# Optimization experiments

Measured on AMD Instinct MI355X. Metric: run time of the kernel, lower is better.

Reference implementation:

```python
import jax, jax.numpy as jnp
import numpy as np

N_NODES = 10000
N_EDGES = 320000
D = 128
H = 4
C = 128
L = 2
NEG_SLOPE = 0.2
LN_EPS = 1e-5


def setup_inputs() -> dict:
    key = jax.random.key(0)
    ks = jax.random.split(key, 8)
    x = jax.random.normal(ks[0], (N_NODES, D), dtype=jnp.float32)
    edge_index = jax.random.randint(ks[1], (2, N_EDGES), 0, N_NODES, dtype=jnp.int64)
    # weights scaled ~Glorot to keep attention logits in a sane range
    Wl = jax.random.normal(ks[2], (L, D, H * C), dtype=jnp.float32) * 0.1
    Wr = jax.random.normal(ks[3], (L, D, H * C), dtype=jnp.float32) * 0.1
    att = jax.random.normal(ks[4], (L, H, C), dtype=jnp.float32) * 0.1
    return {
        "x": x,
        "edge_index": edge_index,
        "Wl": Wl,
        "bl": jnp.zeros((L, H * C), jnp.float32),
        "Wr": Wr,
        "br": jnp.zeros((L, H * C), jnp.float32),
        "att": att,
        "bias": jnp.zeros((L, D), jnp.float32),
        "ln_g": jnp.ones((L, D), jnp.float32),
        "ln_b": jnp.zeros((L, D), jnp.float32),
    }


def _gatv2_layer(x, src, dst, Wl, bl, Wr, br, att, b):
    """GATv2Conv (concat=False -> head mean), messages src->dst, softmax over dst."""
    n = x.shape[0]
    xl = (x @ Wl + bl).reshape(n, H, C)  # source transform
    xr = (x @ Wr + br).reshape(n, H, C)  # target transform
    s = jax.nn.leaky_relu(xl[src] + xr[dst], NEG_SLOPE)  # [E, H, C]
    e = jnp.einsum("ehc,hc->eh", s, att)  # attention logits [E, H]
    m = jax.ops.segment_max(e, dst, num_segments=n)  # stable softmax per dst segment
    ex = jnp.exp(e - m[dst])
    denom = jax.ops.segment_sum(ex, dst, num_segments=n)
    alpha = ex / denom[dst]  # [E, H]
    out = jax.ops.segment_sum(alpha[:, :, None] * xl[src], dst, num_segments=n)  # [N, H, C]
    return out.mean(axis=1) + b  # concat=False -> mean over heads, then bias


def _layer_norm(h, g, b):
    mu = h.mean(-1, keepdims=True)
    var = ((h - mu) ** 2).mean(-1, keepdims=True)
    return (h - mu) * jax.lax.rsqrt(var + LN_EPS) * g + b


def reference(x, edge_index, Wl, bl, Wr, br, att, bias, ln_g, ln_b):
    n = x.shape[0]
    loop = jnp.arange(n, dtype=edge_index.dtype)
    src = jnp.concatenate([edge_index[0], loop])  # add self-loops (PyG default)
    dst = jnp.concatenate([edge_index[1], loop])
    for i in range(L):
        h = _gatv2_layer(x, src, dst, Wl[i], bl[i], Wr[i], br[i], att[i], bias[i])
        x = h + x  # residual
        x = jax.nn.relu(_layer_norm(x, ln_g[i], ln_b[i]))
    return x
```

## Files before the change

kernel.cpp:

```cpp
#include <hip/hip_runtime.h>
#include <math.h>

#define N_NODES 10000
#define N_EDGES 320000
#define E_TOT   (N_EDGES + N_NODES)
#define NEG 0.2f
#define CAP 96

typedef short bf16x8 __attribute__((ext_vector_type(8)));
typedef float f32x4 __attribute__((ext_vector_type(4)));
typedef float f32x2 __attribute__((ext_vector_type(2)));

static __device__ __forceinline__ float4 ld4g(const float* p) { return *(const float4*)p; }

static __device__ __forceinline__ uint4 ldg4(const unsigned short* p, unsigned byteoff) {
    return *(const uint4*)((const char*)p + byteoff);
}
static __device__ __forceinline__ int ldgi(const int* p, int e) { return p[e]; }

static __device__ __forceinline__ unsigned short f2b(float f) {
    unsigned u;
    __builtin_memcpy(&u, &f, 4);
    unsigned r = (u + 0x7fffu + ((u >> 16) & 1u)) >> 16;
    return (unsigned short)r;
}
static __device__ __forceinline__ f32x2 unpk(unsigned d) {
    f32x2 r;
    r.x = __uint_as_float(d << 16);
    r.y = __uint_as_float(d & 0xffff0000u);
    return r;
}

template <int CTRL>
static __device__ __forceinline__ float dpp_add_step(float x) {
    int y = __builtin_amdgcn_update_dpp(0, __float_as_int(x), CTRL, 0xf, 0xf, true);
    return x + __int_as_float(y);
}
static __device__ __forceinline__ float row_sum16(float x) {
    x = dpp_add_step<0x121>(x);
    x = dpp_add_step<0x122>(x);
    x = dpp_add_step<0x124>(x);
    x = dpp_add_step<0x128>(x);
    return x;
}

static __device__ __forceinline__ void comp_full(
    uint4 u,
    const f32x2* __restrict__ xr2, const f32x2* __restrict__ at2,
    f32x2* __restrict__ acc2, float* __restrict__ dsum) {
    const f32x2 neg2 = {NEG, NEG};
    const unsigned* w = (const unsigned*)&u;
    f32x2 F[4];
#pragma unroll
    for (int q = 0; q < 4; ++q) F[q] = unpk(w[q]);
    f32x2 qq = {0.f, 0.f};
#pragma unroll
    for (int q = 0; q < 4; ++q) {
        f32x2 s = F[q] + xr2[q];
        s = __builtin_elementwise_max(s, s * neg2);
        qq = __builtin_elementwise_fma(s, at2[q], qq);
    }
    float ev = __expf(row_sum16(qq.x + qq.y));
    *dsum += ev;
    f32x2 W = {ev, ev};
#pragma unroll
    for (int q = 0; q < 4; ++q)
        acc2[q] = __builtin_elementwise_fma(F[q], W, acc2[q]);
}

static __device__ __forceinline__ void comp_mask(
    uint4 u, bool valid,
    const f32x2* __restrict__ xr2, const f32x2* __restrict__ at2,
    f32x2* __restrict__ acc2, float* __restrict__ dsum) {
    const f32x2 neg2 = {NEG, NEG};
    const unsigned* w = (const unsigned*)&u;
    f32x2 F[4];
#pragma unroll
    for (int q = 0; q < 4; ++q) F[q] = unpk(w[q]);
    f32x2 qq = {0.f, 0.f};
#pragma unroll
    for (int q = 0; q < 4; ++q) {
        f32x2 s = F[q] + xr2[q];
        s = __builtin_elementwise_max(s, s * neg2);
        qq = __builtin_elementwise_fma(s, at2[q], qq);
    }
    float ev = __expf(row_sum16(qq.x + qq.y));
    ev = valid ? ev : 0.f;
    *dsum += ev;
    f32x2 W = {ev, ev};
#pragma unroll
    for (int q = 0; q < 4; ++q)
        acc2[q] = __builtin_elementwise_fma(F[q], W, acc2[q]);
}

__global__ __launch_bounds__(256) void prep_fused_kernel(
    const float* __restrict__ x,
    const float* __restrict__ Wl, const float* __restrict__ Wr,
    unsigned short* __restrict__ xb, unsigned short* __restrict__ WT,
    int* __restrict__ deg) {
    int tid = threadIdx.x, bid = blockIdx.x;
    __shared__ float tbuf[32][33];

    for (int i = bid * 256 + tid; i < N_NODES; i += 256 * 256) deg[i] = 0;

    int l = bid >> 7;
    int rest = bid & 127;
    int ky = rest >> 5, nx = rest & 31;
    int n0 = nx * 32, k0 = ky * 32;
    const float* S = ((n0 < 512) ? Wl : Wr) + (size_t)l * 65536;
    int nn0 = n0 & 511;
    int tx = tid & 31, ty = tid >> 5;
#pragma unroll
    for (int it = 0; it < 4; ++it) {
        int k = k0 + ty + it * 8;
        tbuf[ty + it * 8][tx] = S[(size_t)k * 512 + nn0 + tx];
    }
    __syncthreads();
    unsigned short* dstp = WT + (size_t)l * 1024 * 128;
#pragma unroll
    for (int it = 0; it < 4; ++it) {
        int n = n0 + ty + it * 8;
        int k = k0 + tx;
        dstp[(size_t)n * 128 + k] = f2b(tbuf[tx][ty + it * 8]);
    }
    for (int i = bid * 256 + tid; i < N_NODES * 32; i += 256 * 256) {
        float4 v = ld4g(x + 4 * i);
        ushort4 o = make_ushort4(f2b(v.x), f2b(v.y), f2b(v.z), f2b(v.w));
        *(ushort4*)(xb + 4 * i) = o;
    }
}

template <int DO_FILL>
__global__ __launch_bounds__(256) void gemm_mfma_kernel(const unsigned short* __restrict__ A,
                                                        const unsigned short* __restrict__ Bt,
                                                        const float* __restrict__ bl,
                                                        const float* __restrict__ br,
                                                        unsigned short* __restrict__ xlh,
                                                        unsigned short* __restrict__ xrh,
                                                        const int* __restrict__ ei,
                                                        int* __restrict__ deg,
                                                        int* __restrict__ csr_src) {
    __shared__ unsigned short As[128][72];
    __shared__ unsigned short Bs[128][72];
    int tid = threadIdx.x;
    int wave = tid >> 6, lane = tid & 63;
    int wm = wave >> 1, wn = wave & 1;
    int l15 = lane & 15, quad = lane >> 4;
    int row0 = blockIdx.y * 128, col0 = blockIdx.x * 128;
    const float* bias = (col0 < 512) ? (bl + col0) : (br + col0 - 512);

    f32x4 acc[4][4];
#pragma unroll
    for (int mi = 0; mi < 4; ++mi)
#pragma unroll
        for (int ni = 0; ni < 4; ++ni)
#pragma unroll
            for (int r = 0; r < 4; ++r) acc[mi][ni][r] = 0.f;

#pragma unroll
    for (int kc = 0; kc < 2; ++kc) {
#pragma unroll
        for (int it = 0; it < 4; ++it) {
            int e = tid + it * 256;
            int r = e >> 3, s = e & 7;
            int gr = row0 + r;
            bf16x8 v = (bf16x8)(short)0;
            if (gr < N_NODES) v = *(const bf16x8*)(A + (size_t)gr * 128 + kc * 64 + s * 8);
            *(bf16x8*)&As[r][s * 8] = v;
            bf16x8 w = *(const bf16x8*)(Bt + (size_t)(col0 + r) * 128 + kc * 64 + s * 8);
            *(bf16x8*)&Bs[r][s * 8] = w;
        }
        __syncthreads();
#pragma unroll
        for (int kq = 0; kq < 2; ++kq) {
            bf16x8 af[4], bfr[4];
#pragma unroll
            for (int mi = 0; mi < 4; ++mi)
                af[mi] = *(const bf16x8*)&As[wm * 64 + mi * 16 + l15][kq * 32 + quad * 8];
#pragma unroll
            for (int ni = 0; ni < 4; ++ni)
                bfr[ni] = *(const bf16x8*)&Bs[wn * 64 + ni * 16 + l15][kq * 32 + quad * 8];
#pragma unroll
            for (int mi = 0; mi < 4; ++mi)
#pragma unroll
                for (int ni = 0; ni < 4; ++ni)
                    acc[mi][ni] = __builtin_amdgcn_mfma_f32_16x16x32_bf16(af[mi], bfr[ni], acc[mi][ni], 0, 0, 0);
        }
        __syncthreads();
    }

    float bv[4];
#pragma unroll
    for (int ni = 0; ni < 4; ++ni) bv[ni] = bias[wn * 64 + ni * 16 + l15];

    int h = (col0 >> 7) & 3;
    unsigned short* dstb = ((col0 < 512) ? xlh : xrh) + (((size_t)h * N_NODES) << 7);

#pragma unroll
    for (int mi = 0; mi < 4; ++mi) {
#pragma unroll
        for (int r = 0; r < 4; ++r) {
            int grow = row0 + wm * 64 + mi * 16 + quad * 4 + r;
            if (grow >= N_NODES) continue;
#pragma unroll
            for (int ni = 0; ni < 4; ++ni) {
                int cc = wn * 64 + ni * 16 + l15;
                dstb[((size_t)grow << 7) + cc] = f2b(acc[mi][ni][r] + bv[ni]);
            }
        }
    }

    if (DO_FILL) {
        bool is64 = ((ei[1] | ei[3] | ei[5] | ei[7]) == 0);
        int nthreads = gridDim.x * gridDim.y * 256;
        int gid = (blockIdx.y * gridDim.x + blockIdx.x) * 256 + tid;
        for (int i = gid; i < E_TOT; i += nthreads) {
            int src, dst;
            if (i < N_EDGES) {
                if (is64) { const long long* e = (const long long*)ei; src = (int)e[i]; dst = (int)e[N_EDGES + i]; }
                else { src = ei[i]; dst = ei[N_EDGES + i]; }
            } else {
                src = dst = i - N_EDGES;
            }
            int pos = atomicAdd(&deg[dst], 1);
            if (pos < CAP) csr_src[dst * CAP + pos] = src;
        }
    }
}

__global__ __launch_bounds__(256) void attn_kernel(
    const unsigned short* __restrict__ xlh,
    const unsigned short* __restrict__ xrh,
    const int* __restrict__ deg, const int* __restrict__ csr_src,
    const float* __restrict__ att,
    float* __restrict__ hpart) {
    int tid = threadIdx.x;
    unsigned bid = blockIdx.x;
    int w = tid >> 6, lane = tid & 63;
    int head = __builtin_amdgcn_readfirstlane((int)((bid & 7u) >> 1));
    int slot = (int)((bid >> 3) * 2 + (bid & 1u));
    int e = lane >> 4, g = lane & 15;
    unsigned gboff = (unsigned)(g << 4);

    const unsigned short* XL = xlh + (((size_t)head * N_NODES) << 7);
    const unsigned short* XR = xrh + (((size_t)head * N_NODES) << 7);
    float* HP = hpart + (((size_t)head * N_NODES) << 7);

    f32x2 at2[4];
    {
        const float* ap = att + head * 128 + g * 8;
        float4 a = ld4g(ap);
        float4 b = ld4g(ap + 4);
        at2[0].x = a.x; at2[0].y = a.y; at2[1].x = a.z; at2[1].y = a.w;
        at2[2].x = b.x; at2[2].y = b.y; at2[3].x = b.z; at2[3].y = b.w;
    }

    for (int dst0 = slot * 4 + w; dst0 < N_NODES; dst0 += 2048) {
        int dst = __builtin_amdgcn_readfirstlane(dst0);

        f32x2 xr2[4];
        {
            uint4 u = *(const uint4*)(XR + ((size_t)dst << 7) + g * 8);
            xr2[0] = unpk(u.x); xr2[1] = unpk(u.y); xr2[2] = unpk(u.z); xr2[3] = unpk(u.w);
        }

        int len = deg[dst];
        if (len > CAP) len = CAP;
        const int* cp = csr_src + dst * CAP;
        int full = len >> 2, rem = len & 3;

        float d = 0.f;
        f32x2 acc2[4] = {{0.f, 0.f}, {0.f, 0.f}, {0.f, 0.f}, {0.f, 0.f}};

        if (full) {
            int idx = ldgi(cp, e);
            uint4 uc = ldg4(XL, ((unsigned)idx << 8) + gboff);
            for (int r = 0; r + 1 < full; ++r) {
                int i1 = ldgi(cp + 4 * (r + 1), e);
                uint4 un = ldg4(XL, ((unsigned)i1 << 8) + gboff);
                comp_full(uc, xr2, at2, acc2, &d);
                uc = un;
            }
            comp_full(uc, xr2, at2, acc2, &d);
        }
        if (rem) {
            int raw = ldgi(cp + 4 * full, e);
            int idx = (e < rem) ? raw : 0;
            uint4 u = ldg4(XL, ((unsigned)idx << 8) + gboff);
            comp_mask(u, e < rem, xr2, at2, acc2, &d);
        }

        float t[8];
#pragma unroll
        for (int q = 0; q < 4; ++q) { t[2 * q] = acc2[q].x; t[2 * q + 1] = acc2[q].y; }
#pragma unroll
        for (int j = 0; j < 8; ++j) {
            t[j] += __shfl_xor(t[j], 16, 64);
            t[j] += __shfl_xor(t[j], 32, 64);
        }
        float ds = d;
        ds += __shfl_xor(ds, 16, 64);
        ds += __shfl_xor(ds, 32, 64);
        float inv = 1.f / ds;
#pragma unroll
        for (int j = 0; j < 8; ++j) t[j] *= inv;

        if (lane < 16) {
            float* op = HP + ((size_t)dst << 7) + g * 8;
            *(float4*)op = make_float4(t[0], t[1], t[2], t[3]);
            *(float4*)(op + 4) = make_float4(t[4], t[5], t[6], t[7]);
        }
    }
}

__global__ __launch_bounds__(256) void combine_kernel(
    const float* __restrict__ hpart, const float* __restrict__ x_in,
    const float* __restrict__ bias, const float* __restrict__ ln_g,
    const float* __restrict__ ln_b, float* __restrict__ x_out,
    unsigned short* __restrict__ xb_out) {
    int wv = (blockIdx.x * blockDim.x + threadIdx.x) >> 6;
    if (wv >= N_NODES) return;
    int lane = threadIdx.x & 63;
    int dst = __builtin_amdgcn_readfirstlane(wv);
    int c = lane * 2;
    const float* hp = hpart + ((size_t)dst << 7) + c;
    const size_t hs = ((size_t)N_NODES) << 7;
    f32x2 h0 = *(const f32x2*)(hp);
    f32x2 h1 = *(const f32x2*)(hp + hs);
    f32x2 h2 = *(const f32x2*)(hp + 2 * hs);
    f32x2 h3 = *(const f32x2*)(hp + 3 * hs);
    f32x2 bi = *(const f32x2*)(bias + c);
    f32x2 xi = *(const f32x2*)(x_in + ((size_t)dst << 7) + c);
    f32x2 hc = ((h0 + h1) + (h2 + h3)) * 0.25f + bi + xi;
    float sm = hc.x + hc.y;
    float sq = hc.x * hc.x + hc.y * hc.y;
    sm = row_sum16(sm); sm += __shfl_xor(sm, 16, 64); sm += __shfl_xor(sm, 32, 64);
    sq = row_sum16(sq); sq += __shfl_xor(sq, 16, 64); sq += __shfl_xor(sq, 32, 64);
    float mu = sm * (1.f / 128.f);
    float var = sq * (1.f / 128.f) - mu * mu;
    float rs = rsqrtf(var + 1e-5f);
    f32x2 gg = *(const f32x2*)(ln_g + c);
    f32x2 bb = *(const f32x2*)(ln_b + c);
    float y0 = fmaxf((hc.x - mu) * rs * gg.x + bb.x, 0.f);
    float y1 = fmaxf((hc.y - mu) * rs * gg.y + bb.y, 0.f);
    f32x2 y = {y0, y1};
    *(f32x2*)(x_out + ((size_t)dst << 7) + c) = y;
    if (xb_out) {
        unsigned pk = ((unsigned)f2b(y0)) | (((unsigned)f2b(y1)) << 16);
        *(unsigned*)(xb_out + ((size_t)dst << 7) + c) = pk;
    }
}

extern "C" void kernel_launch(void* const* d_in, const int* in_sizes, int n_in,
                              void* d_out, int out_size, void* d_ws, size_t ws_size,
                              hipStream_t stream) {
    const float* x    = (const float*)d_in[0];
    const int*   ei   = (const int*)d_in[1];
    const float* Wl   = (const float*)d_in[2];
    const float* bl   = (const float*)d_in[3];
    const float* Wr   = (const float*)d_in[4];
    const float* br   = (const float*)d_in[5];
    const float* att  = (const float*)d_in[6];
    const float* bias = (const float*)d_in[7];
    const float* lng  = (const float*)d_in[8];
    const float* lnb  = (const float*)d_in[9];
    float* out = (float*)d_out;

    char* ws = (char*)d_ws;
    unsigned short* xlh = (unsigned short*)ws; ws += (size_t)4 * N_NODES * 128 * 2;
    unsigned short* xrh = (unsigned short*)ws; ws += (size_t)4 * N_NODES * 128 * 2;
    float* hpart = (float*)ws;          ws += (size_t)4 * N_NODES * 128 * 4;
    float* xbuf  = (float*)ws;          ws += (size_t)N_NODES * 128 * 4;
    unsigned short* xb = (unsigned short*)ws; ws += (size_t)N_NODES * 128 * 2;
    unsigned short* WT = (unsigned short*)ws; ws += (size_t)2 * 1024 * 128 * 2;
    int* deg     = (int*)ws;            ws += (size_t)N_NODES * 4;
    int* csr_src = (int*)ws;            ws += (size_t)N_NODES * CAP * 4;

    prep_fused_kernel<<<256, 256, 0, stream>>>(x, Wl, Wr, xb, WT, deg);

    for (int l = 0; l < 2; ++l) {
        const float* xin = (l == 0) ? x : xbuf;
        float* xout = (l == 0) ? xbuf : out;
        unsigned short* xbo = (l == 0) ? xb : (unsigned short*)nullptr;
        if (l == 0)
            gemm_mfma_kernel<1><<<dim3(8, 79), 256, 0, stream>>>(
                xb, WT, bl, br, xlh, xrh, ei, deg, csr_src);
        else
            gemm_mfma_kernel<0><<<dim3(8, 79), 256, 0, stream>>>(
                xb, WT + (size_t)1024 * 128, bl + 512, br + 512, xlh, xrh, ei, deg, csr_src);
        attn_kernel<<<2048, 256, 0, stream>>>(
            xlh, xrh, deg, csr_src, att + (size_t)l * 512, hpart);
        combine_kernel<<<2500, 256, 0, stream>>>(
            hpart, xin, bias + (size_t)l * 128,
            lng + (size_t)l * 128, lnb + (size_t)l * 128, xout, xbo);
    }
}
```

Measured before the change: 216.1 us.

## Shrink GEMM row tile to 64 and stream B fragments from global memory

The projection GEMM now uses 64-row tiles (grid 8x157 instead of 8x79) and stages only the A tile in shared memory, loading it once with a single barrier. Each wave computes a 16x128 slice and reads its B (weight) fragments straight from global memory into registers instead of through an LDS tile. The goal is more blocks for better CU coverage, less LDS and fewer barriers. The cost is redundant global/L2 reads of the weight matrix across row blocks and less register-level reuse of B.

```diff
diff --git a/kernel.cpp b/kernel.cpp
--- a/kernel.cpp
+++ b/kernel.cpp
@@ -140,74 +140,64 @@
                                                         const int* __restrict__ ei,
                                                         int* __restrict__ deg,
                                                         int* __restrict__ csr_src) {
-    __shared__ unsigned short As[128][72];
-    __shared__ unsigned short Bs[128][72];
+    __shared__ unsigned short As[2][64][72];
     int tid = threadIdx.x;
     int wave = tid >> 6, lane = tid & 63;
-    int wm = wave >> 1, wn = wave & 1;
     int l15 = lane & 15, quad = lane >> 4;
-    int row0 = blockIdx.y * 128, col0 = blockIdx.x * 128;
+    int row0 = blockIdx.y * 64, col0 = blockIdx.x * 128;
     const float* bias = (col0 < 512) ? (bl + col0) : (br + col0 - 512);
 
-    f32x4 acc[4][4];
-#pragma unroll
-    for (int mi = 0; mi < 4; ++mi)
-#pragma unroll
-        for (int ni = 0; ni < 4; ++ni)
-#pragma unroll
-            for (int r = 0; r < 4; ++r) acc[mi][ni][r] = 0.f;
+#pragma unroll
+    for (int it = 0; it < 4; ++it) {
+        int e = tid + it * 256;
+        int r = e >> 4, s = e & 15;
+        int gr = row0 + r;
+        bf16x8 v = (bf16x8)(short)0;
+        if (gr < N_NODES) v = *(const bf16x8*)(A + (size_t)gr * 128 + s * 8);
+        *(bf16x8*)&As[s >> 3][r][(s & 7) * 8] = v;
+    }
+    __syncthreads();
+
+    f32x4 acc[8];
+#pragma unroll
+    for (int ni = 0; ni < 8; ++ni)
+#pragma unroll
+        for (int r = 0; r < 4; ++r) acc[ni][r] = 0.f;
+
+    const unsigned short* Bbase = Bt + (size_t)col0 * 128;
+    unsigned bvo = (unsigned)(l15 * 256 + quad * 16);
 
 #pragma unroll
     for (int kc = 0; kc < 2; ++kc) {
 #pragma unroll
-        for (int it = 0; it < 4; ++it) {
-            int e = tid + it * 256;
-            int r = e >> 3, s = e & 7;
-            int gr = row0 + r;
-            bf16x8 v = (bf16x8)(short)0;
-            if (gr < N_NODES) v = *(const bf16x8*)(A + (size_t)gr * 128 + kc * 64 + s * 8);
-            *(bf16x8*)&As[r][s * 8] = v;
-            bf16x8 w = *(const bf16x8*)(Bt + (size_t)(col0 + r) * 128 + kc * 64 + s * 8);
-            *(bf16x8*)&Bs[r][s * 8] = w;
-        }
-        __syncthreads();
-#pragma unroll
         for (int kq = 0; kq < 2; ++kq) {
-            bf16x8 af[4], bfr[4];
-#pragma unroll
-            for (int mi = 0; mi < 4; ++mi)
-                af[mi] = *(const bf16x8*)&As[wm * 64 + mi * 16 + l15][kq * 32 + quad * 8];
-#pragma unroll
-            for (int ni = 0; ni < 4; ++ni)
-                bfr[ni] = *(const bf16x8*)&Bs[wn * 64 + ni * 16 + l15][kq * 32 + quad * 8];
-#pragma unroll
-            for (int mi = 0; mi < 4; ++mi)
-#pragma unroll
-                for (int ni = 0; ni < 4; ++ni)
-                    acc[mi][ni] = __builtin_amdgcn_mfma_f32_16x16x32_bf16(af[mi], bfr[ni], acc[mi][ni], 0, 0, 0);
-        }
-        __syncthreads();
-    }
-
-    float bv[4];
-#pragma unroll
-    for (int ni = 0; ni < 4; ++ni) bv[ni] = bias[wn * 64 + ni * 16 + l15];
+            bf16x8 af = *(const bf16x8*)&As[kc][wave * 16 + l15][kq * 32 + quad * 8];
+            bf16x8 bfr[8];
+#pragma unroll
+            for (int ni = 0; ni < 8; ++ni) {
+                uint4 u = ldg4(Bbase, bvo + (unsigned)(ni * 4096 + kc * 128 + kq * 64));
+                __builtin_memcpy(&bfr[ni], &u, 16);
+            }
+#pragma unroll
+            for (int ni = 0; ni < 8; ++ni)
+                acc[ni] = __builtin_amdgcn_mfma_f32_16x16x32_bf16(af, bfr[ni], acc[ni], 0, 0, 0);
+        }
+    }
+
+    float bv[8];
+#pragma unroll
+    for (int ni = 0; ni < 8; ++ni) bv[ni] = bias[ni * 16 + l15];
 
     int h = (col0 >> 7) & 3;
     unsigned short* dstb = ((col0 < 512) ? xlh : xrh) + (((size_t)h * N_NODES) << 7);
 
 #pragma unroll
-    for (int mi = 0; mi < 4; ++mi) {
-#pragma unroll
-        for (int r = 0; r < 4; ++r) {
-            int grow = row0 + wm * 64 + mi * 16 + quad * 4 + r;
-            if (grow >= N_NODES) continue;
-#pragma unroll
-            for (int ni = 0; ni < 4; ++ni) {
-                int cc = wn * 64 + ni * 16 + l15;
-                dstb[((size_t)grow << 7) + cc] = f2b(acc[mi][ni][r] + bv[ni]);
-            }
-        }
+    for (int r = 0; r < 4; ++r) {
+        int grow = row0 + wave * 16 + quad * 4 + r;
+        if (grow >= N_NODES) continue;
+#pragma unroll
+        for (int ni = 0; ni < 8; ++ni)
+            dstb[((size_t)grow << 7) + ni * 16 + l15] = f2b(acc[ni][r] + bv[ni]);
     }
 
     if (DO_FILL) {
@@ -383,10 +373,10 @@
         float* xout = (l == 0) ? xbuf : out;
         unsigned short* xbo = (l == 0) ? xb : (unsigned short*)nullptr;
         if (l == 0)
-            gemm_mfma_kernel<1><<<dim3(8, 79), 256, 0, stream>>>(
+            gemm_mfma_kernel<1><<<dim3(8, 157), 256, 0, stream>>>(
                 xb, WT, bl, br, xlh, xrh, ei, deg, csr_src);
         else
-            gemm_mfma_kernel<0><<<dim3(8, 79), 256, 0, stream>>>(
+            gemm_mfma_kernel<0><<<dim3(8, 157), 256, 0, stream>>>(
                 xb, WT + (size_t)1024 * 128, bl + 512, br + 512, xlh, xrh, ei, deg, csr_src);
         attn_kernel<<<2048, 256, 0, stream>>>(
             xlh, xrh, deg, csr_src, att + (size_t)l * 512, hpart);
```

Measured after the change: 239.5 us. +10.8%, slower.
